# Performance work log

Measured on AMD Instinct MI355X. Metric: run time of the kernel, lower is better.

## Reference

```python
import jax, jax.numpy as jnp
import numpy as np

N_NODES = 50000
N_EDGES = 800000
DIM = 64
BN_EPS = 1e-5


def setup_inputs() -> dict:
    key = jax.random.key(0)
    ks = jax.random.split(key, 9)
    s = 1.0 / np.sqrt(DIM)
    feature = jax.random.normal(ks[0], (N_NODES, DIM), jnp.float32)
    edge_index = jax.random.randint(ks[1], (2, N_EDGES), 0, N_NODES)
    Wk = jax.random.normal(ks[2], (DIM, DIM), jnp.float32) * s
    Wq = jax.random.normal(ks[3], (DIM, DIM), jnp.float32) * s
    Wv = jax.random.normal(ks[4], (DIM, DIM), jnp.float32) * s
    bk = jax.random.normal(ks[5], (DIM,), jnp.float32) * 0.01
    bq = jax.random.normal(ks[6], (DIM,), jnp.float32) * 0.01
    bv = jax.random.normal(ks[7], (DIM,), jnp.float32) * 0.01
    bias = jax.random.normal(ks[8], (DIM,), jnp.float32) * 0.01
    gamma = jnp.ones((DIM,), jnp.float32)
    beta = jnp.zeros((DIM,), jnp.float32)
    return dict(feature=feature, edge_index=edge_index, Wk=Wk, bk=bk,
                Wq=Wq, bq=bq, Wv=Wv, bv=bv, bias=bias, gamma=gamma, beta=beta)


def reference(feature, edge_index, Wk, bk, Wq, bq, Wv, bv, bias, gamma, beta):
    # Node-level projections (dense GEMMs on [N, D])
    K = feature @ Wk + bk   # applied to x_i (dst)
    Q = feature @ Wq + bq   # applied to x_j (src)
    V = feature @ Wv + bv   # applied to x_j (src)
    src, dst = edge_index[0], edge_index[1]
    # Per-edge gather -> sigmoid gate -> gated message  [E, D]
    eta = jax.nn.sigmoid(K[dst] + Q[src])
    msg = eta * V[src]
    # Scatter-add into destination nodes  [N, D]
    agg = jax.ops.segment_sum(msg, dst, num_segments=feature.shape[0])
    h = agg + bias
    # BatchNorm1d over nodes (batch statistics, biased variance) + ReLU
    mean = jnp.mean(h, axis=0)
    var = jnp.var(h, axis=0)
    h = (h - mean) * jax.lax.rsqrt(var + BN_EPS) * gamma + beta
    return jax.nn.relu(h)
```

## Files before the change

### kernel.cpp

```cpp
#include <hip/hip_runtime.h>
#include <hip/hip_fp16.h>
#include <stdint.h>

#define N_NODES 50000
#define N_EDGES 800000
#define DIM 64
#define BN_EPS 1e-5f
#define CAP 64
#define ZERO_NODE N_NODES
#define POISON 0xAAAAAAAAu

#define NPTILES 391
#define FUSED_BLOCKS 1173

#define NTILES 3125
#define NSTATS_REP 8

typedef _Float16 f16;
typedef __attribute__((ext_vector_type(8))) _Float16 f16x8;
typedef __attribute__((ext_vector_type(4))) float f32x4;

__global__ __launch_bounds__(256) void setup_kernel(
    const float* __restrict__ Wk, const float* __restrict__ Wq,
    const float* __restrict__ Wv, f16* __restrict__ WT16)
{
  const int i = blockIdx.x * 256 + threadIdx.x;
  const int m = i >> 12;
  const int rem = i & 4095;
  const int k = rem >> 6;
  const int c = rem & 63;
  const float* __restrict__ W = (m == 0) ? Wk : (m == 1) ? Wq : Wv;
  WT16[m * 4096 + c * 64 + k] = (f16)W[k * 64 + c];
}

__global__ __launch_bounds__(256, 4) void proj_scatter_kernel(
    const float* __restrict__ feat, const f16* __restrict__ WT16,
    const float* __restrict__ bk, const float* __restrict__ bq,
    const float* __restrict__ bv,
    float* __restrict__ K, __half* __restrict__ QV,
    const int* __restrict__ ei, uint32_t* __restrict__ counts,
    uint16_t* __restrict__ bucket)
{
  const int b = blockIdx.x;
  const int tid = threadIdx.x;
  const int m3 = b % 3;

  if (m3 != 0) {
    const int sid = (b / 3) * 2 + (m3 - 1);
    const int e0 = sid * 1024;
    const int e1 = (e0 + 1024 < N_EDGES) ? e0 + 1024 : N_EDGES;
    const int base = e0 + tid * 4;
    if (base >= e1) return;
    if (base + 4 <= e1) {
      const int4 s4 = *(const int4*)(ei + base);
      const int4 d4 = *(const int4*)(ei + N_EDGES + base);
      const int ss[4] = {s4.x, s4.y, s4.z, s4.w};
      const int dd[4] = {d4.x, d4.y, d4.z, d4.w};
      uint32_t pos[4];
#pragma unroll
      for (int i = 0; i < 4; ++i)
        pos[i] = atomicAdd(&counts[dd[i]], 1u) - POISON;
#pragma unroll
      for (int i = 0; i < 4; ++i)
        if (pos[i] < CAP) bucket[(size_t)dd[i] * CAP + pos[i]] = (uint16_t)ss[i];
    } else {
      for (int e = base; e < e1; ++e) {
        const int src = ei[e];
        const int dst = ei[N_EDGES + e];
        const uint32_t pos = atomicAdd(&counts[dst], 1u) - POISON;
        if (pos < CAP) bucket[(size_t)dst * CAP + pos] = (uint16_t)src;
      }
    }
    return;
  }

  const int tile0 = (b / 3) * 128;
  const int lane = tid & 63;
  const int w = tid >> 6;
  const int nl = lane & 15;
  const int kg = lane >> 4;

  f16x8 fb[2][2];
#pragma unroll
  for (int g2 = 0; g2 < 2; ++g2) {
    const int node = tile0 + w * 32 + g2 * 16 + nl;
    const bool ok = node < N_NODES;
    const float* fp = feat + (size_t)(ok ? node : 0) * DIM;
#pragma unroll
    for (int kk = 0; kk < 2; ++kk) {
      const float4 x0 = ((const float4*)(fp + kk * 32 + kg * 8))[0];
      const float4 x1 = ((const float4*)(fp + kk * 32 + kg * 8))[1];
      f16x8 r;
      r[0] = (f16)x0.x; r[1] = (f16)x0.y; r[2] = (f16)x0.z; r[3] = (f16)x0.w;
      r[4] = (f16)x1.x; r[5] = (f16)x1.y; r[6] = (f16)x1.z; r[7] = (f16)x1.w;
      if (!ok) r = (f16x8)(f16)0.f;
      fb[g2][kk] = r;
    }
  }

#pragma unroll
  for (int m = 0; m < 3; ++m) {
    const f16* __restrict__ wtm = WT16 + m * 4096;
    const float* __restrict__ bb = (m == 0) ? bk : (m == 1) ? bq : bv;

    f16x8 fa[4][2];
#pragma unroll
    for (int nt = 0; nt < 4; ++nt)
#pragma unroll
      for (int kk = 0; kk < 2; ++kk)
        fa[nt][kk] = *(const f16x8*)&wtm[(nt * 16 + nl) * 64 + kk * 32 + kg * 8];
    f32x4 bias[4];
#pragma unroll
    for (int nt = 0; nt < 4; ++nt)
      bias[nt] = *(const f32x4*)&bb[nt * 16 + kg * 4];

#pragma unroll
    for (int g2 = 0; g2 < 2; ++g2) {
      const int node = tile0 + w * 32 + g2 * 16 + nl;
      f32x4 acc[4];
#pragma unroll
      for (int nt = 0; nt < 4; ++nt) acc[nt] = bias[nt];
#pragma unroll
      for (int kk = 0; kk < 2; ++kk)
#pragma unroll
        for (int nt = 0; nt < 4; ++nt)
          acc[nt] = __builtin_amdgcn_mfma_f32_16x16x32_f16(
              fa[nt][kk], fb[g2][kk], acc[nt], 0, 0, 0);

      if (m == 0) {
        if (node < N_NODES) {
#pragma unroll
          for (int nt = 0; nt < 4; ++nt)
            *(f32x4*)&K[node * 64 + nt * 16 + kg * 4] = acc[nt];
        }
      } else {
        if (node <= N_NODES) {
          const int half = (m == 1) ? 0 : 1;
#pragma unroll
          for (int nt = 0; nt < 4; ++nt) {
            union { __half2 h[2]; uint2 u; } pk;
            pk.h[0] = __floats2half2_rn(acc[nt][0], acc[nt][1]);
            pk.h[1] = __floats2half2_rn(acc[nt][2], acc[nt][3]);
            if (node == N_NODES) { pk.u.x = 0u; pk.u.y = 0u; }
            ((uint2*)QV)[node * 32 + (nt * 4 + kg) * 2 + half] = pk.u;
          }
        }
      }
    }
  }
}

__device__ __forceinline__ float4 edge_acc(float4 acc, const float4 k,
                                           const uint4 qv)
{
  union { uint32_t u; __half2 h; } q0, q1, v0, v1;
  q0.u = qv.x; q1.u = qv.y; v0.u = qv.z; v1.u = qv.w;
  const float2 qa = __half22float2(q0.h);
  const float2 qb = __half22float2(q1.h);
  const float2 va = __half22float2(v0.h);
  const float2 vb = __half22float2(v1.h);
  acc.x += va.x * __builtin_amdgcn_rcpf(1.0f + __expf(-(k.x + qa.x)));
  acc.y += va.y * __builtin_amdgcn_rcpf(1.0f + __expf(-(k.y + qa.y)));
  acc.z += vb.x * __builtin_amdgcn_rcpf(1.0f + __expf(-(k.z + qb.x)));
  acc.w += vb.y * __builtin_amdgcn_rcpf(1.0f + __expf(-(k.w + qb.y)));
  return acc;
}

__global__ __launch_bounds__(256) void aggregate_kernel(
    const uint32_t* __restrict__ counts, const uint16_t* __restrict__ bucket,
    const float4* __restrict__ K4, const uint4* __restrict__ QV4,
    float4* __restrict__ agg4, float* __restrict__ stats)
{
  const int tid = threadIdx.x;
  const int row = tid >> 4;
  const int t = tid & 15;
  const int n = blockIdx.x * 16 + row;

  const float4 k = K4[n * 16 + t];
  int deg = (int)(counts[n] - POISON);
  if (deg > CAP) deg = CAP;
  const uint16_t* bp = bucket + (size_t)n * CAP;
  float4 acc = make_float4(0.f, 0.f, 0.f, 0.f);

  for (int j0 = 0; j0 < deg; j0 += 16) {
    const int navail = deg - j0;
    const int s = (t < navail) ? (int)bp[j0 + t] : ZERO_NODE;

    int sA[8]; uint4 qvA[8];
#pragma unroll
    for (int i = 0; i < 8; ++i) sA[i] = __shfl(s, i, 16);
#pragma unroll
    for (int i = 0; i < 8; ++i) qvA[i] = QV4[sA[i] * 16 + t];

    const bool haveB = navail > 8;
    int sB[8]; uint4 qvB[8];
    if (haveB) {
#pragma unroll
      for (int i = 0; i < 8; ++i) sB[i] = __shfl(s, 8 + i, 16);
#pragma unroll
      for (int i = 0; i < 8; ++i) qvB[i] = QV4[sB[i] * 16 + t];
    }

#pragma unroll
    for (int i = 0; i < 8; ++i) acc = edge_acc(acc, k, qvA[i]);
    if (haveB) {
#pragma unroll
      for (int i = 0; i < 8; ++i) acc = edge_acc(acc, k, qvB[i]);
    }
  }
  agg4[n * 16 + t] = acc;

  __shared__ float sred[2][16][DIM + 4];
  float4 pssq;
  pssq.x = acc.x * acc.x; pssq.y = acc.y * acc.y;
  pssq.z = acc.z * acc.z; pssq.w = acc.w * acc.w;
  *(float4*)&sred[0][row][t * 4] = acc;
  *(float4*)&sred[1][row][t * 4] = pssq;
  __syncthreads();
  if (tid < 128) {
    const int s = tid >> 6, c = tid & 63;
    float v = 0.0f;
#pragma unroll
    for (int r = 0; r < 16; ++r) v += sred[s][r][c];
    atomicAdd(&stats[(blockIdx.x & (NSTATS_REP - 1)) * 128 + tid], v);
  }
}

__global__ __launch_bounds__(256) void out_kernel(
    float* __restrict__ out, const float* __restrict__ stats,
    const float* __restrict__ gamma, const float* __restrict__ beta)
{
  __shared__ float sstats[128];
  const int tid = threadIdx.x;
  if (tid < 128) {
    float v = 0.0f;
#pragma unroll
    for (int r = 0; r < NSTATS_REP; ++r) v += stats[r * 128 + tid];
    sstats[tid] = v;
  }
  __syncthreads();

  const int idx = blockIdx.x * 256 + tid;
  if (idx >= N_NODES * (DIM / 4)) return;
  const int t = idx & 15;
  const float4 v = ((const float4*)out)[idx];
  const float invN = 1.0f / (float)N_NODES;
  const float vin[4] = { v.x, v.y, v.z, v.w };
  float o[4];
#pragma unroll
  for (int j = 0; j < 4; ++j) {
    const int c = t * 4 + j;
    const float mean = sstats[c] * invN;
    float var = sstats[DIM + c] * invN - mean * mean;
    var = var < 0.0f ? 0.0f : var;
    const float scale = rsqrtf(var + BN_EPS) * gamma[c];
    const float shift = beta[c] - mean * scale;
    const float x = vin[j] * scale + shift;
    o[j] = x > 0.0f ? x : 0.0f;
  }
  float4 r; r.x = o[0]; r.y = o[1]; r.z = o[2]; r.w = o[3];
  ((float4*)out)[idx] = r;
}

extern "C" void kernel_launch(void* const* d_in, const int* in_sizes, int n_in,
                              void* d_out, int out_size, void* d_ws, size_t ws_size,
                              hipStream_t stream) {
  (void)in_sizes; (void)n_in; (void)out_size; (void)ws_size;
  const float* feat  = (const float*)d_in[0];
  const int*   ei    = (const int*)d_in[1];
  const float* Wk    = (const float*)d_in[2];
  const float* bk    = (const float*)d_in[3];
  const float* Wq    = (const float*)d_in[4];
  const float* bq    = (const float*)d_in[5];
  const float* Wv    = (const float*)d_in[6];
  const float* bv    = (const float*)d_in[7];
  const float* gamma = (const float*)d_in[9];
  const float* beta  = (const float*)d_in[10];

  char* base = (char*)d_ws;
  float*    K      = (float*)base;
  __half*   QV     = (__half*)(base + 12800000);
  float*    stats  = (float*)(base + 25600256);
  f16*      WT16   = (f16*)(base + 25604352);
  uint32_t* counts = (uint32_t*)(base + 25628928);
  uint16_t* bucket = (uint16_t*)(base + 25828928);

  setup_kernel<<<48, 256, 0, stream>>>(Wk, Wq, Wv, WT16);

  proj_scatter_kernel<<<FUSED_BLOCKS, 256, 0, stream>>>(
      feat, WT16, bk, bq, bv, K, QV, ei, counts, bucket);

  aggregate_kernel<<<NTILES, 256, 0, stream>>>(
      counts, bucket, (const float4*)K, (const uint4*)QV, (float4*)d_out,
      stats);

  out_kernel<<<(N_NODES * (DIM / 4) + 255) / 256, 256, 0, stream>>>(
      (float*)d_out, stats, gamma, beta);
}
```

Baseline: 174.9 us.

## Fuse all stages into one cooperative persistent kernel with grid syncs

Replaces the four separate launches (weight transpose, projection+scatter, aggregation, batchnorm output) with a single cooperative kernel of 1024 blocks that separates the phases with grid.sync(). This removes launch gaps and lets blocks stride over aggregation tiles and output elements. The trade-off is that projection no longer overlaps with scatter, only 391 blocks do projection work, and each grid barrier costs time. If the cooperative launch fails, the code falls back to the original four-kernel path.

```diff
diff --git a/kernel.cpp b/kernel.cpp
--- a/kernel.cpp
+++ b/kernel.cpp
@@ -1,6 +1,9 @@
 #include <hip/hip_runtime.h>
 #include <hip/hip_fp16.h>
+#include <hip/hip_cooperative_groups.h>
 #include <stdint.h>
+
+namespace cg = cooperative_groups;
 
 #define N_NODES 50000
 #define N_EDGES 800000
@@ -11,70 +14,64 @@
 #define POISON 0xAAAAAAAAu
 
 #define NPTILES 391
-#define FUSED_BLOCKS 1173
-
+#define NSCAT 782
 #define NTILES 3125
 #define NSTATS_REP 8
+#define COOP_BLOCKS 1024
 
 typedef _Float16 f16;
 typedef __attribute__((ext_vector_type(8))) _Float16 f16x8;
 typedef __attribute__((ext_vector_type(4))) float f32x4;
 
-__global__ __launch_bounds__(256) void setup_kernel(
+
+__device__ __forceinline__ void do_wt16(int gi,
     const float* __restrict__ Wk, const float* __restrict__ Wq,
     const float* __restrict__ Wv, f16* __restrict__ WT16)
 {
-  const int i = blockIdx.x * 256 + threadIdx.x;
-  const int m = i >> 12;
-  const int rem = i & 4095;
+  const int m = gi >> 12;
+  const int rem = gi & 4095;
   const int k = rem >> 6;
   const int c = rem & 63;
   const float* __restrict__ W = (m == 0) ? Wk : (m == 1) ? Wq : Wv;
   WT16[m * 4096 + c * 64 + k] = (f16)W[k * 64 + c];
 }
 
-__global__ __launch_bounds__(256, 4) void proj_scatter_kernel(
+__device__ __forceinline__ void do_scatter(int sid, int tid,
+    const int* __restrict__ ei, uint32_t* __restrict__ counts,
+    uint16_t* __restrict__ bucket)
+{
+  const int e0 = sid * 1024;
+  const int e1 = (e0 + 1024 < N_EDGES) ? e0 + 1024 : N_EDGES;
+  const int base = e0 + tid * 4;
+  if (base + 4 <= e1) {
+    const int4 s4 = *(const int4*)(ei + base);
+    const int4 d4 = *(const int4*)(ei + N_EDGES + base);
+    const int ss[4] = {s4.x, s4.y, s4.z, s4.w};
+    const int dd[4] = {d4.x, d4.y, d4.z, d4.w};
+    uint32_t pos[4];
+#pragma unroll
+    for (int i = 0; i < 4; ++i)
+      pos[i] = atomicAdd(&counts[dd[i]], 1u) - POISON;
+#pragma unroll
+    for (int i = 0; i < 4; ++i)
+      if (pos[i] < CAP) bucket[(size_t)dd[i] * CAP + pos[i]] = (uint16_t)ss[i];
+  } else {
+    for (int e = base; e < e1; ++e) {
+      const int src = ei[e];
+      const int dst = ei[N_EDGES + e];
+      const uint32_t pos = atomicAdd(&counts[dst], 1u) - POISON;
+      if (pos < CAP) bucket[(size_t)dst * CAP + pos] = (uint16_t)src;
+    }
+  }
+}
+
+__device__ __forceinline__ void do_proj(int p, int tid,
     const float* __restrict__ feat, const f16* __restrict__ WT16,
     const float* __restrict__ bk, const float* __restrict__ bq,
     const float* __restrict__ bv,
-    float* __restrict__ K, __half* __restrict__ QV,
-    const int* __restrict__ ei, uint32_t* __restrict__ counts,
-    uint16_t* __restrict__ bucket)
-{
-  const int b = blockIdx.x;
-  const int tid = threadIdx.x;
-  const int m3 = b % 3;
-
-  if (m3 != 0) {
-    const int sid = (b / 3) * 2 + (m3 - 1);
-    const int e0 = sid * 1024;
-    const int e1 = (e0 + 1024 < N_EDGES) ? e0 + 1024 : N_EDGES;
-    const int base = e0 + tid * 4;
-    if (base >= e1) return;
-    if (base + 4 <= e1) {
-      const int4 s4 = *(const int4*)(ei + base);
-      const int4 d4 = *(const int4*)(ei + N_EDGES + base);
-      const int ss[4] = {s4.x, s4.y, s4.z, s4.w};
-      const int dd[4] = {d4.x, d4.y, d4.z, d4.w};
-      uint32_t pos[4];
-#pragma unroll
-      for (int i = 0; i < 4; ++i)
-        pos[i] = atomicAdd(&counts[dd[i]], 1u) - POISON;
-#pragma unroll
-      for (int i = 0; i < 4; ++i)
-        if (pos[i] < CAP) bucket[(size_t)dd[i] * CAP + pos[i]] = (uint16_t)ss[i];
-    } else {
-      for (int e = base; e < e1; ++e) {
-        const int src = ei[e];
-        const int dst = ei[N_EDGES + e];
-        const uint32_t pos = atomicAdd(&counts[dst], 1u) - POISON;
-        if (pos < CAP) bucket[(size_t)dst * CAP + pos] = (uint16_t)src;
-      }
-    }
-    return;
-  }
-
-  const int tile0 = (b / 3) * 128;
+    float* __restrict__ K, __half* __restrict__ QV)
+{
+  const int tile0 = p * 128;
   const int lane = tid & 63;
   const int w = tid >> 6;
   const int nl = lane & 15;
@@ -166,15 +163,15 @@
   return acc;
 }
 
-__global__ __launch_bounds__(256) void aggregate_kernel(
+__device__ __forceinline__ void do_agg_tile(int tile, int tid,
     const uint32_t* __restrict__ counts, const uint16_t* __restrict__ bucket,
     const float4* __restrict__ K4, const uint4* __restrict__ QV4,
-    float4* __restrict__ agg4, float* __restrict__ stats)
-{
-  const int tid = threadIdx.x;
+    float4* __restrict__ agg4, float* __restrict__ stats,
+    float (*sred)[16][DIM + 4])
+{
   const int row = tid >> 4;
   const int t = tid & 15;
-  const int n = blockIdx.x * 16 + row;
+  const int n = tile * 16 + row;
 
   const float4 k = K4[n * 16 + t];
   int deg = (int)(counts[n] - POISON);
@@ -210,7 +207,7 @@
   }
   agg4[n * 16 + t] = acc;
 
-  __shared__ float sred[2][16][DIM + 4];
+  __syncthreads();
   float4 pssq;
   pssq.x = acc.x * acc.x; pssq.y = acc.y * acc.y;
   pssq.z = acc.z * acc.z; pssq.w = acc.w * acc.w;
@@ -222,26 +219,14 @@
     float v = 0.0f;
 #pragma unroll
     for (int r = 0; r < 16; ++r) v += sred[s][r][c];
-    atomicAdd(&stats[(blockIdx.x & (NSTATS_REP - 1)) * 128 + tid], v);
-  }
-}
-
-__global__ __launch_bounds__(256) void out_kernel(
-    float* __restrict__ out, const float* __restrict__ stats,
-    const float* __restrict__ gamma, const float* __restrict__ beta)
-{
-  __shared__ float sstats[128];
-  const int tid = threadIdx.x;
-  if (tid < 128) {
-    float v = 0.0f;
-#pragma unroll
-    for (int r = 0; r < NSTATS_REP; ++r) v += stats[r * 128 + tid];
-    sstats[tid] = v;
-  }
-  __syncthreads();
-
-  const int idx = blockIdx.x * 256 + tid;
-  if (idx >= N_NODES * (DIM / 4)) return;
+    atomicAdd(&stats[(tile & (NSTATS_REP - 1)) * 128 + tid], v);
+  }
+}
+
+__device__ __forceinline__ void do_out_elem(int idx, float* __restrict__ out,
+    const float* __restrict__ sstats, const float* __restrict__ gamma,
+    const float* __restrict__ beta)
+{
   const int t = idx & 15;
   const float4 v = ((const float4*)out)[idx];
   const float invN = 1.0f / (float)N_NODES;
@@ -260,6 +245,97 @@
   }
   float4 r; r.x = o[0]; r.y = o[1]; r.z = o[2]; r.w = o[3];
   ((float4*)out)[idx] = r;
+}
+
+__global__ __launch_bounds__(256, 4) void fused_kernel(
+    const float* __restrict__ feat, const float* __restrict__ Wk,
+    const float* __restrict__ Wq, const float* __restrict__ Wv,
+    const float* __restrict__ bk, const float* __restrict__ bq,
+    const float* __restrict__ bv, const float* __restrict__ gamma,
+    const float* __restrict__ beta, const int* __restrict__ ei,
+    float* __restrict__ out, float* __restrict__ K, __half* __restrict__ QV,
+    f16* __restrict__ WT16, uint32_t* __restrict__ counts,
+    uint16_t* __restrict__ bucket, float* __restrict__ stats)
+{
+  __shared__ float sred[2][16][DIM + 4];
+  __shared__ float sstats[128];
+  cg::grid_group grid = cg::this_grid();
+  const int bid = blockIdx.x;
+  const int tid = threadIdx.x;
+
+  {
+    const int gi = bid * 256 + tid;
+    if (gi < 3 * 64 * 64) do_wt16(gi, Wk, Wq, Wv, WT16);
+    if (bid < NSCAT) do_scatter(bid, tid, ei, counts, bucket);
+  }
+  grid.sync();
+
+  if (bid < NPTILES) do_proj(bid, tid, feat, WT16, bk, bq, bv, K, QV);
+  grid.sync();
+
+  for (int tile = bid; tile < NTILES; tile += COOP_BLOCKS)
+    do_agg_tile(tile, tid, counts, bucket, (const float4*)K,
+                (const uint4*)QV, (float4*)out, stats, sred);
+  grid.sync();
+
+  if (tid < 128) {
+    float v = 0.0f;
+#pragma unroll
+    for (int r = 0; r < NSTATS_REP; ++r) v += stats[r * 128 + tid];
+    sstats[tid] = v;
+  }
+  __syncthreads();
+  for (int idx = bid * 256 + tid; idx < N_NODES * (DIM / 4);
+       idx += COOP_BLOCKS * 256)
+    do_out_elem(idx, out, sstats, gamma, beta);
+}
+
+__global__ __launch_bounds__(256) void setup_kernel(
+    const float* __restrict__ Wk, const float* __restrict__ Wq,
+    const float* __restrict__ Wv, f16* __restrict__ WT16)
+{
+  const int gi = blockIdx.x * 256 + threadIdx.x;
+  if (gi < 3 * 64 * 64) do_wt16(gi, Wk, Wq, Wv, WT16);
+}
+
+__global__ __launch_bounds__(256, 4) void ps_kernel(
+    const float* __restrict__ feat, const f16* __restrict__ WT16,
+    const float* __restrict__ bk, const float* __restrict__ bq,
+    const float* __restrict__ bv, float* __restrict__ K,
+    __half* __restrict__ QV, const int* __restrict__ ei,
+    uint32_t* __restrict__ counts, uint16_t* __restrict__ bucket)
+{
+  const int b = blockIdx.x;
+  const int m3 = b % 3;
+  if (m3 != 0) do_scatter((b / 3) * 2 + (m3 - 1), threadIdx.x, ei, counts, bucket);
+  else do_proj(b / 3, threadIdx.x, feat, WT16, bk, bq, bv, K, QV);
+}
+
+__global__ __launch_bounds__(256) void agg_kernel(
+    const uint32_t* __restrict__ counts, const uint16_t* __restrict__ bucket,
+    const float4* __restrict__ K4, const uint4* __restrict__ QV4,
+    float4* __restrict__ agg4, float* __restrict__ stats)
+{
+  __shared__ float sred[2][16][DIM + 4];
+  do_agg_tile(blockIdx.x, threadIdx.x, counts, bucket, K4, QV4, agg4, stats,
+              sred);
+}
+
+__global__ __launch_bounds__(256) void out_kernel(
+    float* __restrict__ out, const float* __restrict__ stats,
+    const float* __restrict__ gamma, const float* __restrict__ beta)
+{
+  __shared__ float sstats[128];
+  const int tid = threadIdx.x;
+  if (tid < 128) {
+    float v = 0.0f;
+#pragma unroll
+    for (int r = 0; r < NSTATS_REP; ++r) v += stats[r * 128 + tid];
+    sstats[tid] = v;
+  }
+  __syncthreads();
+  const int idx = blockIdx.x * 256 + tid;
+  if (idx < N_NODES * (DIM / 4)) do_out_elem(idx, out, sstats, gamma, beta);
 }
 
 extern "C" void kernel_launch(void* const* d_in, const int* in_sizes, int n_in,
@@ -276,6 +352,7 @@
   const float* bv    = (const float*)d_in[7];
   const float* gamma = (const float*)d_in[9];
   const float* beta  = (const float*)d_in[10];
+  float* out = (float*)d_out;
 
   char* base = (char*)d_ws;
   float*    K      = (float*)base;
@@ -285,15 +362,23 @@
   uint32_t* counts = (uint32_t*)(base + 25628928);
   uint16_t* bucket = (uint16_t*)(base + 25828928);
 
-  setup_kernel<<<48, 256, 0, stream>>>(Wk, Wq, Wv, WT16);
-
-  proj_scatter_kernel<<<FUSED_BLOCKS, 256, 0, stream>>>(
-      feat, WT16, bk, bq, bv, K, QV, ei, counts, bucket);
-
-  aggregate_kernel<<<NTILES, 256, 0, stream>>>(
-      counts, bucket, (const float4*)K, (const uint4*)QV, (float4*)d_out,
-      stats);
-
-  out_kernel<<<(N_NODES * (DIM / 4) + 255) / 256, 256, 0, stream>>>(
-      (float*)d_out, stats, gamma, beta);
-}
+  void* args[] = {
+    (void*)&feat, (void*)&Wk, (void*)&Wq, (void*)&Wv,
+    (void*)&bk, (void*)&bq, (void*)&bv, (void*)&gamma, (void*)&beta,
+    (void*)&ei, (void*)&out, (void*)&K, (void*)&QV, (void*)&WT16,
+    (void*)&counts, (void*)&bucket, (void*)&stats
+  };
+  const hipError_t err = hipLaunchCooperativeKernel(
+      (const void*)fused_kernel, dim3(COOP_BLOCKS), dim3(256), args, 0, stream);
+
+  if (err != hipSuccess) {
+    setup_kernel<<<48, 256, 0, stream>>>(Wk, Wq, Wv, WT16);
+    ps_kernel<<<1173, 256, 0, stream>>>(feat, WT16, bk, bq, bv, K, QV, ei,
+                                        counts, bucket);
+    agg_kernel<<<NTILES, 256, 0, stream>>>(counts, bucket, (const float4*)K,
+                                           (const uint4*)QV, (float4*)out,
+                                           stats);
+    out_kernel<<<(N_NODES * (DIM / 4) + 255) / 256, 256, 0, stream>>>(
+        out, stats, gamma, beta);
+  }
+}
```

Measured after the change: 547.1 us. 3.13x slower.
